# Kernel tuning notes

Hardware: AMD Instinct MI355X
Metric: run time of the kernel (lower is better)

The kernel has to match this reference:

```python
import jax, jax.numpy as jnp
import numpy as np

B, T, I, H = 64, 1024, 256, 512
CLIP = 5.0


def setup_inputs() -> dict:
    key = jax.random.key(0)
    k0, k1, k2, k3 = jax.random.split(key, 4)
    x = jax.random.normal(k0, (B, T, I), dtype=jnp.float32)
    h0 = 0.1 * jax.random.normal(k1, (B, H), dtype=jnp.float32)
    # scale=True: ih_scale = I*(I+H)/I = I+H ; hh_scale = H*(I+H)/H = I+H
    std = 1.0 / np.sqrt(np.float32(I + H))
    W_ih = std * jax.random.normal(k2, (3 * H, I), dtype=jnp.float32)
    W_hh = std * jax.random.normal(k3, (3 * H, H), dtype=jnp.float32)
    # bias_ih: ones, last H entries zeroed; bias_hh: zeros (frozen)
    b_ih = jnp.concatenate([jnp.ones(2 * H, jnp.float32), jnp.zeros(H, jnp.float32)])
    b_hh = jnp.zeros(3 * H, jnp.float32)
    return {"x": x, "h0": h0, "W_ih": W_ih, "b_ih": b_ih, "W_hh": W_hh, "b_hh": b_hh}


def reference(x, h0, W_ih, b_ih, W_hh, b_hh):
    # Precompute input projections for all timesteps (same math, batched GEMM)
    x_all = jnp.einsum('bti,gi->btg', x, W_ih) + b_ih  # [B,T,3H]
    x_z, x_r, x_n = jnp.split(x_all, 3, axis=-1)       # each [B,T,H]
    W_zr, W_n = W_hh[: 2 * H], W_hh[2 * H:]
    b_zr, b_n = b_hh[: 2 * H], b_hh[2 * H:]

    def step(h, xs):
        xz, xr, xn = xs                                 # each [B,H]
        h_all = h @ W_zr.T + b_zr                       # [B,2H]
        hz, hr = jnp.split(h_all, 2, axis=-1)
        z = jax.nn.sigmoid(xz + hz)
        r = jax.nn.sigmoid(xr + hr)
        hn = (r * h) @ W_n.T + b_n
        n = jnp.tanh(xn + hn)
        h_new = jnp.clip(z * h + (1.0 - z) * n, -CLIP, CLIP)
        return h_new, h_new

    xs = (jnp.swapaxes(x_z, 0, 1), jnp.swapaxes(x_r, 0, 1), jnp.swapaxes(x_n, 0, 1))
    h_last, hs = jax.lax.scan(step, h0, xs)             # hs: [T,B,H]
    return jnp.swapaxes(hs, 0, 1), h_last
```

## Files before the change

kernel.cpp:

```cpp
#include <hip/hip_runtime.h>

#define BB   64
#define TT   1024
#define II   256
#define HH   512
#define NBLK 32
#define NTHR 512
#define SLICE 16
#define WHH_STR 520
#define WIH_STR 264
#define CLIPV 5.0f

typedef __attribute__((ext_vector_type(8))) short short8;
typedef __attribute__((ext_vector_type(4))) float f32x4;

__device__ __forceinline__ unsigned short f2bf(float f){
    unsigned u = __float_as_uint(f);
    u += 0x7fffu + ((u >> 16) & 1u);
    return (unsigned short)(u >> 16);
}
__device__ __forceinline__ float bf2f(unsigned short s){
    return __uint_as_float(((unsigned)s) << 16);
}
__device__ __forceinline__ unsigned packsplit(float f){
    unsigned short hi = f2bf(f);
    unsigned short lo = f2bf(f - bf2f(hi));
    return (unsigned)hi | ((unsigned)lo << 16);
}

__device__ __forceinline__ void unpack8(const uint4 a, const uint4 b, short8 &hi, short8 &lo){
    hi[0]=(short)a.x; lo[0]=(short)(a.x>>16);
    hi[1]=(short)a.y; lo[1]=(short)(a.y>>16);
    hi[2]=(short)a.z; lo[2]=(short)(a.z>>16);
    hi[3]=(short)a.w; lo[3]=(short)(a.w>>16);
    hi[4]=(short)b.x; lo[4]=(short)(b.x>>16);
    hi[5]=(short)b.y; lo[5]=(short)(b.y>>16);
    hi[6]=(short)b.z; lo[6]=(short)(b.z>>16);
    hi[7]=(short)b.w; lo[7]=(short)(b.w>>16);
}

#define SPLIT1(f, j) { float f_=(f); unsigned short h_=f2bf(f_); hi[j]=(short)h_; lo[j]=(short)f2bf(f_-bf2f(h_)); }
__device__ __forceinline__ void split8(const float4 a, const float4 b, short8 &hi, short8 &lo){
    SPLIT1(a.x,0) SPLIT1(a.y,1) SPLIT1(a.z,2) SPLIT1(a.w,3)
    SPLIT1(b.x,4) SPLIT1(b.y,5) SPLIT1(b.z,6) SPLIT1(b.w,7)
}
#undef SPLIT1

__device__ __forceinline__ f32x4 mfma(short8 a, short8 b, f32x4 c){
    return __builtin_amdgcn_mfma_f32_16x16x32_bf16(a, b, c, 0, 0, 0);
}

__device__ __forceinline__ void wait_flags(const unsigned* f, unsigned target){
    int lane = threadIdx.x & 63;
    const unsigned* p = f + (lane & 31);
    while (true){
        unsigned v = __hip_atomic_load(p, __ATOMIC_ACQUIRE, __HIP_MEMORY_SCOPE_AGENT);
        if (__all((int)(v >= target))) break;
        __builtin_amdgcn_s_sleep(1);
    }
}

#define LDS_BYTES ((48*WHH_STR + 48*WIH_STR)*2*2 + 64*4 + 1024*4)

extern "C" __global__ void pack_x_kernel(const float* __restrict__ x,
                                         unsigned* __restrict__ xp, int n){
    int idx = blockIdx.x * 256 + threadIdx.x;
    if (idx < n) xp[idx] = packsplit(x[idx]);
}

extern "C" __global__ void __launch_bounds__(NTHR, 2) gru_scan(
    const float* __restrict__ x,  const float* __restrict__ h0,
    const float* __restrict__ Wih, const float* __restrict__ bih,
    const float* __restrict__ Whh, const float* __restrict__ bhh,
    float* __restrict__ out, unsigned* __restrict__ ws,
    const unsigned* __restrict__ xp)
{
    extern __shared__ char smem[];
    unsigned short* whh_hi = (unsigned short*)smem;
    unsigned short* whh_lo = whh_hi + 48*WHH_STR;
    unsigned short* wih_hi = whh_lo + 48*WHH_STR;
    unsigned short* wih_lo = wih_hi + 48*WIH_STR;
    float* biasL = (float*)(wih_lo + 48*WIH_STR);
    float* nh1   = biasL + 64;

    unsigned* flagA = ws;
    unsigned* flagB = ws + 32;
    unsigned* hp    = ws + 128;
    unsigned* rhp   = hp + BB*HH;

    const int tid = threadIdx.x;
    const int bb  = blockIdx.x;
    const int colBase = SLICE * bb;

    for (int e = tid; e < 48*HH; e += NTHR){
        int r = e >> 9, k = e & (HH-1);
        int g = r >> 4, j = r & 15;
        int grow = g*HH + colBase + j;
        float v = Whh[grow*HH + k];
        unsigned short hv = f2bf(v);
        whh_hi[r*WHH_STR + k] = hv;
        whh_lo[r*WHH_STR + k] = f2bf(v - bf2f(hv));
    }
    for (int e = tid; e < 48*II; e += NTHR){
        int r = e >> 8, k = e & (II-1);
        int g = r >> 4, j = r & 15;
        int grow = g*HH + colBase + j;
        float v = Wih[grow*II + k];
        unsigned short hv = f2bf(v);
        wih_hi[r*WIH_STR + k] = hv;
        wih_lo[r*WIH_STR + k] = f2bf(v - bf2f(hv));
    }
    if (tid < 48){
        int g = tid >> 4, j = tid & 15;
        int grow = g*HH + colBase + j;
        biasL[tid] = bih[grow] + bhh[grow];
    }
    for (int e = tid; e < BB*SLICE; e += NTHR){
        int m = e >> 4, c = e & 15;
        hp[m*HH + colBase + c] = packsplit(h0[m*HH + colBase + c]);
    }
    __syncthreads();
    if (tid == 0) __hip_atomic_fetch_add(flagB + bb, 1u, __ATOMIC_RELEASE, __HIP_MEMORY_SCOPE_AGENT);

    const int w = tid >> 6, lane = tid & 63;
    const int quad = lane >> 4, li = lane & 15;
    const int g = w >> 2, mt = w & 3;
    const int am  = mt*16 + li;
    const int cg  = colBase + li;
    const int dm0 = mt*16 + quad*4;

    float zh[4], omz[4];
    f32x4 accNX;

    for (int t = 0; t < TT; ++t){
        uint4 xbuf[16];
        {
            const char* xb;
            if (xp) xb = (const char*)(xp + ((size_t)am*TT + t)*II + quad*8);
            else    xb = (const char*)(x  + ((size_t)am*TT + t)*II + quad*8);
            #pragma unroll
            for (int kt = 0; kt < 8; ++kt){
                xbuf[2*kt]   = *(const uint4*)(xb + (size_t)kt*128);
                xbuf[2*kt+1] = *(const uint4*)(xb + (size_t)kt*128 + 16);
            }
        }
        wait_flags(flagB, (unsigned)(t+1));

        f32x4 accG = {0.f,0.f,0.f,0.f};
        accNX = (f32x4){0.f,0.f,0.f,0.f};
        #pragma unroll
        for (int kt = 0; kt < 8; ++kt){
            short8 ah, al;
            if (xp) unpack8(xbuf[2*kt], xbuf[2*kt+1], ah, al);
            else {
                float4 f0 = *(const float4*)&xbuf[2*kt];
                float4 f1 = *(const float4*)&xbuf[2*kt+1];
                split8(f0, f1, ah, al);
            }
            int ko = kt*32 + quad*8;
            short8 bh = *(const short8*)(wih_hi + (g*16+li)*WIH_STR + ko);
            short8 bl = *(const short8*)(wih_lo + (g*16+li)*WIH_STR + ko);
            accG = mfma(ah, bh, accG);
            accG = mfma(ah, bl, accG);
            accG = mfma(al, bh, accG);
            if (g == 0){
                short8 nbh = *(const short8*)(wih_hi + (32+li)*WIH_STR + ko);
                short8 nbl = *(const short8*)(wih_lo + (32+li)*WIH_STR + ko);
                accNX = mfma(ah, nbh, accNX);
                accNX = mfma(ah, nbl, accNX);
                accNX = mfma(al, nbh, accNX);
            }
        }
        #pragma unroll
        for (int kt = 0; kt < 16; ++kt){
            int ko = kt*32 + quad*8;
            uint4 p0 = *(const uint4*)(hp + am*HH + ko);
            uint4 p1 = *(const uint4*)(hp + am*HH + ko + 4);
            short8 ah, al; unpack8(p0, p1, ah, al);
            short8 bh = *(const short8*)(whh_hi + (g*16+li)*WHH_STR + ko);
            short8 bl = *(const short8*)(whh_lo + (g*16+li)*WHH_STR + ko);
            accG = mfma(ah, bh, accG);
            accG = mfma(ah, bl, accG);
            accG = mfma(al, bh, accG);
        }
        {
            float bsum = biasL[g*16 + li];
            #pragma unroll
            for (int i = 0; i < 4; ++i){
                unsigned ph = hp[(dm0+i)*HH + cg];
                float hvf = bf2f((unsigned short)ph) + bf2f((unsigned short)(ph>>16));
                float gate = 1.f/(1.f + __expf(-(accG[i] + bsum)));
                if (g == 0){ zh[i] = gate*hvf; omz[i] = 1.f - gate; }
                else       { rhp[(dm0+i)*HH + cg] = packsplit(gate*hvf); }
            }
        }
        __syncthreads();
        if (tid == 0) __hip_atomic_fetch_add(flagA + bb, 1u, __ATOMIC_RELEASE, __HIP_MEMORY_SCOPE_AGENT);

        wait_flags(flagA, (unsigned)(t+1));
        f32x4 accN = (g == 0) ? accNX : (f32x4){0.f,0.f,0.f,0.f};
        #pragma unroll
        for (int kt8 = 0; kt8 < 8; ++kt8){
            int kt = g*8 + kt8;
            int ko = kt*32 + quad*8;
            uint4 p0 = *(const uint4*)(rhp + am*HH + ko);
            uint4 p1 = *(const uint4*)(rhp + am*HH + ko + 4);
            short8 ah, al; unpack8(p0, p1, ah, al);
            short8 bh = *(const short8*)(whh_hi + (32+li)*WHH_STR + ko);
            short8 bl = *(const short8*)(whh_lo + (32+li)*WHH_STR + ko);
            accN = mfma(ah, bh, accN);
            accN = mfma(ah, bl, accN);
            accN = mfma(al, bh, accN);
        }
        if (g == 1){
            #pragma unroll
            for (int i = 0; i < 4; ++i) nh1[(dm0+i)*16 + li] = accN[i];
        }
        __syncthreads();
        if (g == 0){
            float bn = biasL[32 + li];
            #pragma unroll
            for (int i = 0; i < 4; ++i){
                float np = accN[i] + nh1[(dm0+i)*16 + li] + bn;
                float n  = tanhf(np);
                float hv = zh[i] + omz[i]*n;
                hv = fminf(fmaxf(hv, -CLIPV), CLIPV);
                out[((size_t)(dm0+i)*TT + t)*HH + cg] = hv;
                if (t == TT-1) out[(size_t)BB*TT*HH + (size_t)(dm0+i)*HH + cg] = hv;
                hp[(dm0+i)*HH + cg] = packsplit(hv);
            }
        }
        __syncthreads();
        if (tid == 0) __hip_atomic_fetch_add(flagB + bb, 1u, __ATOMIC_RELEASE, __HIP_MEMORY_SCOPE_AGENT);
    }
}

extern "C" void kernel_launch(void* const* d_in, const int* in_sizes, int n_in,
                              void* d_out, int out_size, void* d_ws, size_t ws_size,
                              hipStream_t stream) {
    const float* x   = (const float*)d_in[0];
    const float* h0  = (const float*)d_in[1];
    const float* Wih = (const float*)d_in[2];
    const float* bih = (const float*)d_in[3];
    const float* Whh = (const float*)d_in[4];
    const float* bhh = (const float*)d_in[5];
    float* out = (float*)d_out;
    unsigned* ws = (unsigned*)d_ws;

    const size_t base_bytes = 512 + 2*(size_t)BB*HH*4;
    const size_t xp_bytes   = (size_t)BB*TT*II*4;
    unsigned* xp = nullptr;
    if (ws_size >= base_bytes + xp_bytes){
        xp = ws + base_bytes/4;
        int n = BB*TT*II;
        pack_x_kernel<<<dim3((n + 255)/256), dim3(256), 0, stream>>>(x, xp, n);
    }
    hipMemsetAsync(d_ws, 0, 512, stream);
    (void)hipFuncSetAttribute((const void*)gru_scan,
                              hipFuncAttributeMaxDynamicSharedMemorySize,
                              (int)LDS_BYTES);
    gru_scan<<<dim3(NBLK), dim3(NTHR), LDS_BYTES, stream>>>(
        x, h0, Wih, bih, Whh, bhh, out, ws, xp);
}
```

Before: 26.40 ms.

## Replace block barriers with per-wave relaxed flags and keep own h slice locally

Removes the __syncthreads barriers around the cross-block flag signals. Each of the 8 waves now drains its own memory ops and bumps the flag with a relaxed atomic, and waiters expect 8 increments per step. The sleep in the spin loop and the acquire/release ordering are dropped. The x-projection MFMAs are moved ahead of the flag wait so they overlap it, h loads become 64-bit relaxed atomics into registers, and the block's own h slice is kept in LDS and registers instead of being re-read from global. Launch bounds change from 2 to 1 blocks per CU. Relying on relaxed atomics plus s_waitcnt for cross-CU visibility risks memory-ordering bugs.

```diff
diff --git a/kernel.cpp b/kernel.cpp
--- a/kernel.cpp
+++ b/kernel.cpp
@@ -13,6 +13,7 @@
 
 typedef __attribute__((ext_vector_type(8))) short short8;
 typedef __attribute__((ext_vector_type(4))) float f32x4;
+typedef unsigned long long u64;
 
 __device__ __forceinline__ unsigned short f2bf(float f){
     unsigned u = __float_as_uint(f);
@@ -50,17 +51,32 @@
     return __builtin_amdgcn_mfma_f32_16x16x32_bf16(a, b, c, 0, 0, 0);
 }
 
+__device__ __forceinline__ u64 ld64(const u64* p){
+    return __hip_atomic_load((u64*)p, __ATOMIC_RELAXED, __HIP_MEMORY_SCOPE_AGENT);
+}
+__device__ __forceinline__ void st32(unsigned* p, unsigned v){
+    __hip_atomic_store(p, v, __ATOMIC_RELAXED, __HIP_MEMORY_SCOPE_AGENT);
+}
+__device__ __forceinline__ unsigned ldflag(const unsigned* p){
+    return __hip_atomic_load((unsigned*)p, __ATOMIC_RELAXED, __HIP_MEMORY_SCOPE_AGENT);
+}
+__device__ __forceinline__ void addflag(unsigned* p){
+    __hip_atomic_fetch_add(p, 1u, __ATOMIC_RELAXED, __HIP_MEMORY_SCOPE_AGENT);
+}
+__device__ __forceinline__ void drain(){
+    asm volatile("s_waitcnt vmcnt(0) lgkmcnt(0)" ::: "memory");
+}
+
 __device__ __forceinline__ void wait_flags(const unsigned* f, unsigned target){
-    int lane = threadIdx.x & 63;
-    const unsigned* p = f + (lane & 31);
+    const unsigned* p = f + (threadIdx.x & 31);
     while (true){
-        unsigned v = __hip_atomic_load(p, __ATOMIC_ACQUIRE, __HIP_MEMORY_SCOPE_AGENT);
+        unsigned v = ldflag(p);
         if (__all((int)(v >= target))) break;
-        __builtin_amdgcn_s_sleep(1);
-    }
-}
-
-#define LDS_BYTES ((48*WHH_STR + 48*WIH_STR)*2*2 + 64*4 + 1024*4)
+    }
+    asm volatile("" ::: "memory");
+}
+
+#define LDS_BYTES ((48*WHH_STR + 48*WIH_STR)*2*2 + 64*4 + 1024*4 + 1024*4)
 
 extern "C" __global__ void pack_x_kernel(const float* __restrict__ x,
                                          unsigned* __restrict__ xp, int n){
@@ -68,7 +84,7 @@
     if (idx < n) xp[idx] = packsplit(x[idx]);
 }
 
-extern "C" __global__ void __launch_bounds__(NTHR, 2) gru_scan(
+extern "C" __global__ void __launch_bounds__(NTHR, 1) gru_scan(
     const float* __restrict__ x,  const float* __restrict__ h0,
     const float* __restrict__ Wih, const float* __restrict__ bih,
     const float* __restrict__ Whh, const float* __restrict__ bhh,
@@ -82,6 +98,7 @@
     unsigned short* wih_lo = wih_hi + 48*WIH_STR;
     float* biasL = (float*)(wih_lo + 48*WIH_STR);
     float* nh1   = biasL + 64;
+    float* h_own = nh1 + 1024;
 
     unsigned* flagA = ws;
     unsigned* flagB = ws + 32;
@@ -117,10 +134,12 @@
     }
     for (int e = tid; e < BB*SLICE; e += NTHR){
         int m = e >> 4, c = e & 15;
-        hp[m*HH + colBase + c] = packsplit(h0[m*HH + colBase + c]);
+        float v = h0[m*HH + colBase + c];
+        st32(hp + m*HH + colBase + c, packsplit(v));
+        h_own[m*16 + c] = v;
     }
     __syncthreads();
-    if (tid == 0) __hip_atomic_fetch_add(flagB + bb, 1u, __ATOMIC_RELEASE, __HIP_MEMORY_SCOPE_AGENT);
+    if ((tid & 63) == 0) addflag(flagB + bb);
 
     const int w = tid >> 6, lane = tid & 63;
     const int quad = lane >> 4, li = lane & 15;
@@ -129,12 +148,18 @@
     const int cg  = colBase + li;
     const int dm0 = mt*16 + quad*4;
 
+    float hprev[4];
+    #pragma unroll
+    for (int i = 0; i < 4; ++i) hprev[i] = h0[(size_t)(dm0+i)*HH + cg];
+
     float zh[4], omz[4];
     f32x4 accNX;
 
     for (int t = 0; t < TT; ++t){
-        uint4 xbuf[16];
+        f32x4 accG = {0.f,0.f,0.f,0.f};
+        accNX = (f32x4){0.f,0.f,0.f,0.f};
         {
+            uint4 xbuf[16];
             const char* xb;
             if (xp) xb = (const char*)(xp + ((size_t)am*TT + t)*II + quad*8);
             else    xb = (const char*)(x  + ((size_t)am*TT + t)*II + quad*8);
@@ -143,74 +168,103 @@
                 xbuf[2*kt]   = *(const uint4*)(xb + (size_t)kt*128);
                 xbuf[2*kt+1] = *(const uint4*)(xb + (size_t)kt*128 + 16);
             }
-        }
-        wait_flags(flagB, (unsigned)(t+1));
-
-        f32x4 accG = {0.f,0.f,0.f,0.f};
-        accNX = (f32x4){0.f,0.f,0.f,0.f};
-        #pragma unroll
-        for (int kt = 0; kt < 8; ++kt){
-            short8 ah, al;
-            if (xp) unpack8(xbuf[2*kt], xbuf[2*kt+1], ah, al);
-            else {
-                float4 f0 = *(const float4*)&xbuf[2*kt];
-                float4 f1 = *(const float4*)&xbuf[2*kt+1];
-                split8(f0, f1, ah, al);
-            }
-            int ko = kt*32 + quad*8;
-            short8 bh = *(const short8*)(wih_hi + (g*16+li)*WIH_STR + ko);
-            short8 bl = *(const short8*)(wih_lo + (g*16+li)*WIH_STR + ko);
-            accG = mfma(ah, bh, accG);
-            accG = mfma(ah, bl, accG);
-            accG = mfma(al, bh, accG);
-            if (g == 0){
-                short8 nbh = *(const short8*)(wih_hi + (32+li)*WIH_STR + ko);
-                short8 nbl = *(const short8*)(wih_lo + (32+li)*WIH_STR + ko);
-                accNX = mfma(ah, nbh, accNX);
-                accNX = mfma(ah, nbl, accNX);
-                accNX = mfma(al, nbh, accNX);
-            }
-        }
-        #pragma unroll
-        for (int kt = 0; kt < 16; ++kt){
-            int ko = kt*32 + quad*8;
-            uint4 p0 = *(const uint4*)(hp + am*HH + ko);
-            uint4 p1 = *(const uint4*)(hp + am*HH + ko + 4);
-            short8 ah, al; unpack8(p0, p1, ah, al);
-            short8 bh = *(const short8*)(whh_hi + (g*16+li)*WHH_STR + ko);
-            short8 bl = *(const short8*)(whh_lo + (g*16+li)*WHH_STR + ko);
-            accG = mfma(ah, bh, accG);
-            accG = mfma(ah, bl, accG);
-            accG = mfma(al, bh, accG);
+            #pragma unroll
+            for (int kt = 0; kt < 8; ++kt){
+                short8 ah, al;
+                if (xp) unpack8(xbuf[2*kt], xbuf[2*kt+1], ah, al);
+                else {
+                    float4 f0 = *(const float4*)&xbuf[2*kt];
+                    float4 f1 = *(const float4*)&xbuf[2*kt+1];
+                    split8(f0, f1, ah, al);
+                }
+                int ko = kt*32 + quad*8;
+                short8 bh = *(const short8*)(wih_hi + (g*16+li)*WIH_STR + ko);
+                short8 bl = *(const short8*)(wih_lo + (g*16+li)*WIH_STR + ko);
+                accG = mfma(ah, bh, accG);
+                accG = mfma(ah, bl, accG);
+                accG = mfma(al, bh, accG);
+                if (g == 0){
+                    short8 nbh = *(const short8*)(wih_hi + (32+li)*WIH_STR + ko);
+                    short8 nbl = *(const short8*)(wih_lo + (32+li)*WIH_STR + ko);
+                    accNX = mfma(ah, nbh, accNX);
+                    accNX = mfma(ah, nbl, accNX);
+                    accNX = mfma(al, nbh, accNX);
+                }
+            }
+        }
+
+        wait_flags(flagB, (unsigned)(8*(t+1)));
+
+        {
+            u64 hb[64];
+            const u64* hrow = (const u64*)(hp + (size_t)am*HH) + quad*4;
+            #pragma unroll
+            for (int k4 = 0; k4 < 64; ++k4){
+                int kt = k4 >> 2, j = k4 & 3;
+                hb[k4] = ld64(hrow + kt*16 + j);
+            }
+            #pragma unroll
+            for (int kt = 0; kt < 16; ++kt){
+                short8 ah, al;
+                #pragma unroll
+                for (int j = 0; j < 4; ++j){
+                    u64 v = hb[kt*4+j];
+                    unsigned d0 = (unsigned)v, d1 = (unsigned)(v >> 32);
+                    ah[2*j]   = (short)d0;  al[2*j]   = (short)(d0 >> 16);
+                    ah[2*j+1] = (short)d1;  al[2*j+1] = (short)(d1 >> 16);
+                }
+                int ko = kt*32 + quad*8;
+                short8 bh = *(const short8*)(whh_hi + (g*16+li)*WHH_STR + ko);
+                short8 bl = *(const short8*)(whh_lo + (g*16+li)*WHH_STR + ko);
+                accG = mfma(ah, bh, accG);
+                accG = mfma(ah, bl, accG);
+                accG = mfma(al, bh, accG);
+            }
         }
         {
             float bsum = biasL[g*16 + li];
             #pragma unroll
             for (int i = 0; i < 4; ++i){
-                unsigned ph = hp[(dm0+i)*HH + cg];
-                float hvf = bf2f((unsigned short)ph) + bf2f((unsigned short)(ph>>16));
                 float gate = 1.f/(1.f + __expf(-(accG[i] + bsum)));
-                if (g == 0){ zh[i] = gate*hvf; omz[i] = 1.f - gate; }
-                else       { rhp[(dm0+i)*HH + cg] = packsplit(gate*hvf); }
-            }
-        }
-        __syncthreads();
-        if (tid == 0) __hip_atomic_fetch_add(flagA + bb, 1u, __ATOMIC_RELEASE, __HIP_MEMORY_SCOPE_AGENT);
-
-        wait_flags(flagA, (unsigned)(t+1));
+                if (g == 0){
+                    zh[i] = gate*hprev[i]; omz[i] = 1.f - gate;
+                } else {
+                    float hvf = h_own[(dm0+i)*16 + li];
+                    st32(rhp + (size_t)(dm0+i)*HH + cg, packsplit(gate*hvf));
+                }
+            }
+        }
+        drain();
+        if (lane == 0) addflag(flagA + bb);
+
+        wait_flags(flagA, (unsigned)(8*(t+1)));
         f32x4 accN = (g == 0) ? accNX : (f32x4){0.f,0.f,0.f,0.f};
-        #pragma unroll
-        for (int kt8 = 0; kt8 < 8; ++kt8){
-            int kt = g*8 + kt8;
-            int ko = kt*32 + quad*8;
-            uint4 p0 = *(const uint4*)(rhp + am*HH + ko);
-            uint4 p1 = *(const uint4*)(rhp + am*HH + ko + 4);
-            short8 ah, al; unpack8(p0, p1, ah, al);
-            short8 bh = *(const short8*)(whh_hi + (32+li)*WHH_STR + ko);
-            short8 bl = *(const short8*)(whh_lo + (32+li)*WHH_STR + ko);
-            accN = mfma(ah, bh, accN);
-            accN = mfma(ah, bl, accN);
-            accN = mfma(al, bh, accN);
+        {
+            u64 rb[32];
+            const u64* rrow = (const u64*)(rhp + (size_t)am*HH) + quad*4 + (size_t)g*8*16;
+            #pragma unroll
+            for (int k4 = 0; k4 < 32; ++k4){
+                int kt8 = k4 >> 2, j = k4 & 3;
+                rb[k4] = ld64(rrow + kt8*16 + j);
+            }
+            #pragma unroll
+            for (int kt8 = 0; kt8 < 8; ++kt8){
+                short8 ah, al;
+                #pragma unroll
+                for (int j = 0; j < 4; ++j){
+                    u64 v = rb[kt8*4+j];
+                    unsigned d0 = (unsigned)v, d1 = (unsigned)(v >> 32);
+                    ah[2*j]   = (short)d0;  al[2*j]   = (short)(d0 >> 16);
+                    ah[2*j+1] = (short)d1;  al[2*j+1] = (short)(d1 >> 16);
+                }
+                int kt = g*8 + kt8;
+                int ko = kt*32 + quad*8;
+                short8 bh = *(const short8*)(whh_hi + (32+li)*WHH_STR + ko);
+                short8 bl = *(const short8*)(whh_lo + (32+li)*WHH_STR + ko);
+                accN = mfma(ah, bh, accN);
+                accN = mfma(ah, bl, accN);
+                accN = mfma(al, bh, accN);
+            }
         }
         if (g == 1){
             #pragma unroll
@@ -227,11 +281,13 @@
                 hv = fminf(fmaxf(hv, -CLIPV), CLIPV);
                 out[((size_t)(dm0+i)*TT + t)*HH + cg] = hv;
                 if (t == TT-1) out[(size_t)BB*TT*HH + (size_t)(dm0+i)*HH + cg] = hv;
-                hp[(dm0+i)*HH + cg] = packsplit(hv);
-            }
-        }
-        __syncthreads();
-        if (tid == 0) __hip_atomic_fetch_add(flagB + bb, 1u, __ATOMIC_RELEASE, __HIP_MEMORY_SCOPE_AGENT);
+                st32(hp + (size_t)(dm0+i)*HH + cg, packsplit(hv));
+                h_own[(dm0+i)*16 + li] = hv;
+                hprev[i] = hv;
+            }
+        }
+        drain();
+        if (lane == 0) addflag(flagB + bb);
     }
 }
 
```

Measured after the change: 37.10 ms. +40.5%, slower.
